# Kernel tuning notes

Measured on AMD Instinct MI355X. Metric: run time of the kernel, lower is better.

The kernel has to match this reference:

```python
import jax, jax.numpy as jnp
import numpy as np

B, CIN, H, W = 8, 128, 32, 32
COUT, K, STRIDE, PAD = 128, 3, 1, 1
DK, DV, NH = 64, 64, 8
DKH, DVH = DK // NH, DV // NH


def conv2d(x, w, b, stride, pad):
    out = jax.lax.conv_general_dilated(
        x, w, (stride, stride), [(pad, pad), (pad, pad)],
        dimension_numbers=("NCHW", "OIHW", "NCHW"))
    return out + b[None, :, None, None]


def rel_to_abs(x):
    # x: (b, Nh, L, 2L-1) relative -> (b, Nh, L, L) absolute via pad/reshape/slice
    b, nh, L, _ = x.shape
    x = jnp.pad(x, ((0, 0), (0, 0), (0, 0), (0, 1)))          # (b,Nh,L,2L)
    flat = x.reshape(b, nh, L * 2 * L)
    flat = jnp.pad(flat, ((0, 0), (0, 0), (0, L - 1)))
    final = flat.reshape(b, nh, L + 1, 2 * L - 1)
    return final[:, :, :L, L - 1:]


def relative_logits_1d(q, key_rel, Hh, Ww, Nh, case):
    # q: (b, Nh, x, y, dkh); key_rel: (2*len-1, dkh)
    rel = jnp.einsum("bhxyd,md->bhxym", q, key_rel)
    rel = rel.reshape(-1, Nh * Hh, Ww, 2 * Ww - 1)
    rel = rel_to_abs(rel)
    rel = rel.reshape(-1, Nh, Hh, Ww, Ww)
    rel = jnp.tile(rel[:, :, :, None, :, :], (1, 1, 1, Hh, 1, 1))  # (b,Nh,H,H,W,W)
    if case == "h":
        # torch .transpose(2,4).transpose(3,5)
        rel = rel.transpose(0, 1, 4, 5, 2, 3)
    return rel.reshape(-1, Nh, Hh * Ww, Hh * Ww)


def reference(x, w_general, b_general, w_qkv, b_qkv, w_out, b_out, key_rel_h, key_rel_w):
    batch, _, height, width = x.shape
    conv_out = conv2d(x, w_general, b_general, STRIDE, PAD)

    qkv = conv2d(x, w_qkv, b_qkv, 1, 0)
    q, k, v = jnp.split(qkv, [DK, 2 * DK], axis=1)
    # split heads: (B, Nh, c//Nh, H, W)
    q = q.reshape(batch, NH, DKH, height, width)
    k = k.reshape(batch, NH, DKH, height, width)
    v = v.reshape(batch, NH, DVH, height, width)
    # faithful to original bug: q / dkh**(-0.5) == q * sqrt(dkh)
    q = q / (DKH ** (-0.5))

    flat_q = q.reshape(batch, NH, height * width, DKH)
    flat_k = k.reshape(batch, NH, height * width, DKH)
    flat_v = v.reshape(batch, NH, height * width, DVH)

    logits = jnp.einsum("bhnd,bhmd->bhnm", flat_q, flat_k)

    # relative position logits
    q5 = q.transpose(0, 1, 3, 4, 2)  # (B, Nh, H, W, dkh)
    logits = logits + relative_logits_1d(q5, key_rel_h, height, width, NH, "h")
    logits = logits + relative_logits_1d(q5.transpose(0, 1, 3, 2, 4), key_rel_w, height, width, NH, "w")

    weights = jax.nn.softmax(logits, axis=-1)
    attn = jnp.einsum("bhnm,bhmd->bhnd", weights, flat_v)
    attn = attn.reshape(batch, NH, height, width, DVH)
    # combine heads: (B, Nh*dvh, H, W)
    attn = attn.transpose(0, 1, 4, 2, 3).reshape(batch, NH * DVH, height, width)
    attn = conv2d(attn, w_out, b_out, STRIDE, PAD)
    return jnp.concatenate((conv_out, attn), axis=1)


def setup_inputs():
    key = jax.random.key(0)
    ks = jax.random.split(key, 8)
    f = jnp.float32
    x = jax.random.normal(ks[0], (B, CIN, H, W), f)
    w_general = jax.random.normal(ks[1], (COUT - DV, CIN, K, K), f) * 0.02
    b_general = jnp.zeros((COUT - DV,), f)
    w_qkv = jax.random.normal(ks[2], (2 * DK + DV, CIN, 1, 1), f) * 0.05
    b_qkv = jnp.zeros((2 * DK + DV,), f)
    w_out = jax.random.normal(ks[3], (DV, DV, K, K), f) * 0.05
    b_out = jnp.zeros((DV,), f)
    key_rel_h = jax.random.normal(ks[4], (2 * H - 1, DKH), f)
    key_rel_w = jax.random.normal(ks[5], (2 * W - 1, DKH), f)
    return {"x": x, "w_general": w_general, "b_general": b_general,
            "w_qkv": w_qkv, "b_qkv": b_qkv, "w_out": w_out, "b_out": b_out,
            "key_rel_h": key_rel_h, "key_rel_w": key_rel_w}
```

## Files before the change

kernel.cpp:

```cpp
#include <hip/hip_runtime.h>
#include <hip/hip_bf16.h>


#define NP 1024
#define QSCALE 2.8284271247461903f
#define LOG2E  1.4426950408889634f

using bf16 = __hip_bfloat16;
typedef unsigned short ushort;
typedef unsigned int uint;
using bf16x8 = __attribute__((ext_vector_type(8))) short;
using f32x4  = __attribute__((ext_vector_type(4))) float;
using f32x2  = __attribute__((ext_vector_type(2))) float;

__device__ __forceinline__ float b2f(bf16 v) { return __bfloat162float(v); }
__device__ __forceinline__ ushort f2b(float v) {
  bf16 h = __float2bfloat16(v);
  ushort u; __builtin_memcpy(&u, &h, 2); return u;
}
__device__ __forceinline__ f32x2 up2(uint u) {
  f32x2 r;
  r[0] = __uint_as_float(u << 16);
  r[1] = __uint_as_float(u & 0xffff0000u);
  return r;
}

__device__ __forceinline__ float dot8(const float* a, const float* b) {
  float s = a[0] * b[0];
  s = fmaf(a[1], b[1], s); s = fmaf(a[2], b[2], s); s = fmaf(a[3], b[3], s);
  s = fmaf(a[4], b[4], s); s = fmaf(a[5], b[5], s); s = fmaf(a[6], b[6], s);
  s = fmaf(a[7], b[7], s);
  return s;
}

__device__ __forceinline__ int fenc(float f) { int i = __float_as_int(f); return i < 0 ? (i ^ 0x7fffffff) : i; }
__device__ __forceinline__ float fdec(int i) { return __int_as_float(i < 0 ? (i ^ 0x7fffffff) : i); }

#if defined(__has_builtin)
#if __has_builtin(__builtin_amdgcn_exp2f)
#define EXP2F __builtin_amdgcn_exp2f
#else
#define EXP2F exp2f
#endif
#else
#define EXP2F exp2f
#endif

#define OFF_QBUF   0
#define OFF_KB16   524288
#define OFF_VTB    786432
#define OFF_XPB    1310720
#define OFF_APB    1902592
#define OFF_WGB    2198528
#define OFF_WOB    2235392
#define OFF_BG     2253824
#define OFF_BQKV   2253888
#define OFF_BO     2254080
#define OFF_KRH    2254144
#define OFF_KRW    2254648
#define OFF_FLAG   2255152
#define OFF_WQB    2255168

__global__ __launch_bounds__(256) void cvt_kernel(
    const void* __restrict__ p0, const void* __restrict__ p1, const void* __restrict__ p2,
    const void* __restrict__ p3, const void* __restrict__ p4, const void* __restrict__ p5,
    const void* __restrict__ p6, const void* __restrict__ p7, const void* __restrict__ p8,
    float* __restrict__ ws, int* __restrict__ flag)
{
  __shared__ int partial[4];
  __shared__ uint lds[64][65];
  int t = threadIdx.x;
  const unsigned* xraw = (const unsigned*)p0;
  int cnt = 0;
  for (int i = t; i < 1024; i += 256) {
    unsigned elo = (xraw[i] >> 7) & 0xffu;
    cnt += (elo >= 64u && elo <= 133u) ? 1 : 0;
  }
#pragma unroll
  for (int off = 1; off < 64; off <<= 1) cnt += __shfl_xor(cnt, off);
  if ((t & 63) == 0) partial[t >> 6] = cnt;
  __syncthreads();
  int tot = partial[0] + partial[1] + partial[2] + partial[3];
  int f32 = (tot >= 650) ? 0 : 1;
  if (blockIdx.x == 0 && t == 0) *flag = f32;

  int gsz = gridDim.x * 256;
  int gid = blockIdx.x * 256 + t;

  const void* src[5] = {p2, p4, p6, p7, p8};
  const int   n[5]    = {64, 192, 64, 504, 504};
  const int   doff[5] = {OFF_BG, OFF_BQKV, OFF_BO, OFF_KRH, OFF_KRW};
#pragma unroll
  for (int s = 0; s < 5; s++) {
    float* dst = ws + doff[s];
    if (f32) { const float* sp = (const float*)src[s];
      for (int i = gid; i < n[s]; i += gsz) dst[i] = sp[i];
    } else { const bf16* sp = (const bf16*)src[s];
      for (int i = gid; i < n[s]; i += gsz) dst[i] = b2f(sp[i]);
    }
  }

  {
    float4* z = (float4*)(ws + OFF_VTB);
    for (int i = gid; i < 131072; i += gsz) z[i] = float4{0.f, 0.f, 0.f, 0.f};
  }

  {
    uint4 z = {0u, 0u, 0u, 0u};
    uint4* xp = (uint4*)(ws + OFF_XPB);
    uint4* ap = (uint4*)(ws + OFF_APB);
    for (int s = gid; s < 9248; s += gsz) {
      int pb = s / 1156, rem = s - pb * 1156;
      int y = rem / 34, x = rem - y * 34;
      if (y == 0 || y == 33 || x == 0 || x == 33) {
        uint4* d1 = xp + (size_t)s * 16;
#pragma unroll
        for (int k = 0; k < 16; k++) d1[k] = z;
        uint4* d2 = ap + (size_t)s * 8;
#pragma unroll
        for (int k = 0; k < 8; k++) d2[k] = z;
      }
    }
  }

  {
    ushort* wgb = (ushort*)(ws + OFF_WGB);
    for (int s = gid; s < 73728; s += gsz) {
      int kykx = s >> 13, co = (s >> 7) & 63, ci = s & 127;
      int si = (co * 128 + ci) * 9 + kykx;
      wgb[s] = f32 ? f2b(((const float*)p1)[si]) : ((const ushort*)p1)[si];
    }
  }
  {
    ushort* wob = (ushort*)(ws + OFF_WOB);
    for (int s = gid; s < 36864; s += gsz) {
      int kykx = s >> 12, co = (s >> 6) & 63, ci = s & 63;
      int si = (co * 64 + ci) * 9 + kykx;
      wob[s] = f32 ? f2b(((const float*)p5)[si]) : ((const ushort*)p5)[si];
    }
  }
  {
    ushort* wqb = (ushort*)(ws + OFF_WQB);
    for (int s = gid; s < 24576; s += gsz) {
      wqb[s] = f32 ? f2b(((const float*)p3)[s]) : ((const ushort*)p3)[s];
    }
  }

  if (blockIdx.x < 128) {
    int w = t >> 6, lane = t & 63;
    int b = blockIdx.x >> 4;
    int pp0 = (blockIdx.x & 15) * 64;
    if (f32) {
      const float* xs = (const float*)p0 + (size_t)b * 131072 + pp0;
#pragma unroll 4
      for (int i = 0; i < 16; i++) {
        int cp = w * 16 + i;
        float v0 = xs[(size_t)(2 * cp) * 1024 + lane];
        float v1 = xs[(size_t)(2 * cp + 1) * 1024 + lane];
        lds[cp][lane] = (uint)f2b(v0) | ((uint)f2b(v1) << 16);
      }
    } else {
      const ushort* xs = (const ushort*)p0 + (size_t)b * 131072 + pp0;
#pragma unroll 4
      for (int i = 0; i < 16; i++) {
        int cp = w * 16 + i;
        uint v0 = xs[(size_t)(2 * cp) * 1024 + lane];
        uint v1 = xs[(size_t)(2 * cp + 1) * 1024 + lane];
        lds[cp][lane] = v0 | (v1 << 16);
      }
    }
    __syncthreads();
    uint* xp32 = (uint*)(ws + OFF_XPB);
#pragma unroll 4
    for (int i = 0; i < 16; i++) {
      int p = w * 16 + i;
      int pp = pp0 + p;
      int y = pp >> 5, x = pp & 31;
      xp32[((size_t)(b * 34 + y + 1) * 34 + x + 1) * 64 + lane] = lds[lane][p];
    }
  }
}

__global__ __launch_bounds__(256) void qkv_mfma_kernel(
    const ushort* __restrict__ xp, const ushort* __restrict__ wqb,
    const float* __restrict__ bias, float* __restrict__ qbuf,
    ushort* __restrict__ kb16, ushort* __restrict__ vtb)
{
  int pt = blockIdx.x;
  int b  = blockIdx.y;
  int lane = threadIdx.x & 63;
  int w = threadIdx.x >> 6;
  int n = lane & 15;
  int kg = lane >> 4;
  int p0 = pt * 16;
  int px = p0 + n;
  int y = px >> 5, x = px & 31;

  const ushort* bbase = xp + ((size_t)(b * 34 + y + 1) * 34 + (x + 1)) * 128 + kg * 8;
  bf16x8 Bf[4];
#pragma unroll
  for (int c = 0; c < 4; c++) Bf[c] = *(const bf16x8*)(bbase + c * 32);

  f32x4 acc0 = {0.f, 0.f, 0.f, 0.f};
  f32x4 acc1 = {0.f, 0.f, 0.f, 0.f};
  f32x4 acc2 = {0.f, 0.f, 0.f, 0.f};
  {
    const ushort* abase = wqb + (size_t)(w * 16 + n) * 128 + kg * 8;
#pragma unroll
    for (int c = 0; c < 4; c++) {
      bf16x8 A = *(const bf16x8*)(abase + c * 32);
      acc0 = __builtin_amdgcn_mfma_f32_16x16x32_bf16(A, Bf[c], acc0, 0, 0, 0);
    }
  }
  {
    const ushort* abase = wqb + (size_t)((w + 4) * 16 + n) * 128 + kg * 8;
#pragma unroll
    for (int c = 0; c < 4; c++) {
      bf16x8 A = *(const bf16x8*)(abase + c * 32);
      acc1 = __builtin_amdgcn_mfma_f32_16x16x32_bf16(A, Bf[c], acc1, 0, 0, 0);
    }
  }
  {
    const ushort* abase = wqb + (size_t)((w + 8) * 16 + n) * 128 + kg * 8;
#pragma unroll
    for (int c = 0; c < 4; c++) {
      bf16x8 A = *(const bf16x8*)(abase + c * 32);
      acc2 = __builtin_amdgcn_mfma_f32_16x16x32_bf16(A, Bf[c], acc2, 0, 0, 0);
    }
  }

#pragma unroll
  for (int r = 0; r < 4; r++) {
    int co = w * 16 + kg * 4 + r;
    float v = acc0[r] + bias[co];
    qbuf[((size_t)b * 64 + co) * NP + px] = v * QSCALE;
  }
#pragma unroll
  for (int r = 0; r < 4; r++) {
    int co = (w + 4) * 16 + kg * 4 + r;
    float v = acc1[r] + bias[co];
    kb16[((size_t)b * 64 + (co - 64)) * NP + px] = f2b(v);
  }
#pragma unroll
  for (int r = 0; r < 4; r++) {
    int co = (w + 8) * 16 + kg * 4 + r;
    float v = acc2[r] + bias[co];
    int ch = co - 128;
    int h = ch >> 3;
    int d0 = px & 7;
    int m  = (ch & 7) * 128 + (px >> 3);
    vtb[((size_t)(b * 8 + h) * 16 + d0) * 1024 + m] = f2b(v);
  }
}

template <int CINT>
__device__ __forceinline__ void conv_body(
    const ushort* __restrict__ xp, const ushort* __restrict__ wp,
    const float* __restrict__ bias, void* __restrict__ out,
    int co_base, const int* __restrict__ flag, int pt, int b)
{
  int lane = threadIdx.x & 63;
  int w = threadIdx.x >> 6;
  int n = lane & 15;
  int kg = lane >> 4;
  int p0 = pt * 16;
  int y = p0 >> 5, x0 = p0 & 31;

  const ushort* abase = wp + (size_t)(w * 16 + n) * CINT + kg * 8;
  const ushort* bbase = xp + ((size_t)(b * 34 + y) * 34 + x0 + n) * CINT + kg * 8;

  f32x4 acc0 = {0.f, 0.f, 0.f, 0.f};
  f32x4 acc1 = {0.f, 0.f, 0.f, 0.f};
#pragma unroll
  for (int c = 0; c < CINT / 32; c++) {
    int ci0 = c * 32;
#pragma unroll
    for (int kp = 0; kp < 9; kp++) {
      int ky = kp / 3, kx = kp - ky * 3;
      bf16x8 A = *(const bf16x8*)(abase + (size_t)kp * 64 * CINT + ci0);
      bf16x8 B = *(const bf16x8*)(bbase + (size_t)(ky * 34 + kx) * CINT + ci0);
      if (kp & 1) acc1 = __builtin_amdgcn_mfma_f32_16x16x32_bf16(A, B, acc1, 0, 0, 0);
      else        acc0 = __builtin_amdgcn_mfma_f32_16x16x32_bf16(A, B, acc0, 0, 0, 0);
    }
  }

  int f32o = *flag;
#pragma unroll
  for (int r = 0; r < 4; r++) {
    int co = w * 16 + kg * 4 + r;
    float v = acc0[r] + acc1[r] + bias[co];
    size_t eoff = ((size_t)b * 128 + co_base + co) * 1024 + p0 + n;
    if (f32o) ((float*)out)[eoff] = v;
    else ((bf16*)out)[eoff] = __float2bfloat16(v);
  }
}

__global__ __launch_bounds__(256, 4) void attn_conv_kernel(
    const float* __restrict__ qbuf, const ushort* __restrict__ kb16, const ushort* __restrict__ vtb,
    const float* __restrict__ krh, const float* __restrict__ krw,
    ushort* __restrict__ apb,
    const ushort* __restrict__ xp, const ushort* __restrict__ wgb,
    const float* __restrict__ bg, void* __restrict__ out, const int* __restrict__ flag)
{
  int bx = blockIdx.x;
  if (bx >= 1024) {
    int id = bx - 1024;
    conv_body<128>(xp, wgb, bg, out, 0, flag, id & 63, id >> 6);
    return;
  }

  __shared__ float bw2[2][NP];
  __shared__ float bhT[2][32][32];
  __shared__ float qsT[2][32][8];
  __shared__ __align__(16) float krhs[64][12];
  __shared__ __align__(16) float krws[64][12];
  __shared__ ushort Plds[4][16][40];
  __shared__ float lred[4][16];
  __shared__ int smax[3];

  int t = threadIdx.x;
  int cp = bx & 15, h = (bx >> 4) & 7, b = bx >> 7;
  int C0 = cp * 2;
  const float* qbase = qbuf + ((size_t)b * 64 + h * 8) * NP;
  const uint4* kb4 = (const uint4*)(kb16 + ((size_t)b * 64 + h * 8) * NP);
  const ushort* vth = vtb + (size_t)(b * 8 + h) * 16384;

  if (t < 3) smax[t] = (t == 0) ? 0 : fenc(-3.0e38f);

  for (int idx = t; idx < 63 * 8; idx += 256) {
    krhs[idx >> 3][idx & 7] = krh[idx];
    krws[idx >> 3][idx & 7] = krw[idx];
  }
  for (int idx = t; idx < 512; idx += 256) {
    int cs = idx >> 8, d = (idx >> 5) & 7, r = idx & 31;
    qsT[cs][r][d] = qbase[(size_t)d * NP + r * 32 + (C0 + cs)];
  }
  float kn2 = 0.f;
#pragma unroll
  for (int rr = 0; rr < 4; rr++) {
    uint4 ku = kb4[rr * 256 + t];
    f32x2 k0 = up2(ku.x), k1 = up2(ku.y), k2 = up2(ku.z), k3 = up2(ku.w);
    f32x2 s2 = k0 * k0;
    s2 = __builtin_elementwise_fma(k1, k1, s2);
    s2 = __builtin_elementwise_fma(k2, k2, s2);
    s2 = __builtin_elementwise_fma(k3, k3, s2);
    kn2 = fmaxf(kn2, s2[0] + s2[1]);
  }
  __syncthreads();
  atomicMax(&smax[0], __float_as_int(kn2));

  float bwm = -3.0e38f;
  for (int idx = t; idx < 2048; idx += 256) {
    int cs = idx >> 10, m = idx & 1023;
    int rg = m >> 5, j2 = m & 31;
    float s = dot8(qsT[cs][rg], krws[j2 - rg + 31]) * LOG2E;
    bw2[cs][m] = s;
    bwm = fmaxf(bwm, s);
  }
  float bhm = -3.0e38f;
  for (int idx = t; idx < 2048; idx += 256) {
    int cs = idx >> 10, r = idx & 1023;
    int i = r >> 5, J = r & 31;
    float s = dot8(qsT[cs][i], krhs[J - (C0 + cs) + 31]) * LOG2E;
    bhT[cs][i][J] = s;
    bhm = fmaxf(bhm, s);
  }
  atomicMax(&smax[1], fenc(bwm));
  atomicMax(&smax[2], fenc(bhm));
  __syncthreads();

  float kmaxn = sqrtf(__int_as_float(smax[0]));
  float bmax = fdec(smax[1]) + fdec(smax[2]);

  int w = t >> 6, lane = t & 63;
  int quad = lane >> 4, nIdx = lane & 15;
  int n0 = cp * 64 + w * 16;
  int nQ = n0 + nIdx;
  int Cs = w >> 1;
  int J = ((w & 1) << 4) + nIdx;

  const bf16x8 zero8 = {0, 0, 0, 0, 0, 0, 0, 0};

  const float* qrow = qbase + (size_t)nQ * 8;
  bf16x8 Bq = zero8;
  float nn = 0.f;
  ushort ub[8];
#pragma unroll
  for (int d = 0; d < 8; d++) {
    float v = qrow[d] * LOG2E;
    ub[d] = f2b(v);
    float vr = __uint_as_float((uint)ub[d] << 16);
    nn = fmaf(vr, vr, nn);
  }
  if (quad == 0) {
#pragma unroll
    for (int d = 0; d < 8; d++) Bq[d] = (short)ub[d];
  }
  float Mn = sqrtf(nn) * kmaxn + bmax;

  f32x4 accO = {0.f, 0.f, 0.f, 0.f};
  float lpart = 0.f;
  ushort* prow = &Plds[w][nIdx][0];

#pragma unroll 2
  for (int mc = 0; mc < 32; ++mc) {
    int mb = mc * 32;
    float pre = bhT[Cs][mc][J] - Mn;
    ushort pb[8];
#pragma unroll
    for (int s = 0; s < 2; ++s) {
      int mt = mb + s * 16;
      bf16x8 Ak = *(const bf16x8*)(kb4 + mt + nIdx);
      if (quad != 0) Ak = zero8;
      f32x4 S = __builtin_amdgcn_mfma_f32_16x16x32_bf16(Ak, Bq, f32x4{0.f,0.f,0.f,0.f}, 0, 0, 0);
      float4 bw4 = *(const float4*)&bw2[Cs][mt + (quad << 2)];
      const float bwv[4] = {bw4.x, bw4.y, bw4.z, bw4.w};
#pragma unroll
      for (int r = 0; r < 4; ++r) {
        float p = EXP2F(S[r] + bwv[r] + pre);
        lpart += p;
        pb[s * 4 + r] = f2b(p);
      }
    }
    uint2 w0, w1;
    w0.x = (uint)pb[0] | ((uint)pb[1] << 16);
    w0.y = (uint)pb[2] | ((uint)pb[3] << 16);
    w1.x = (uint)pb[4] | ((uint)pb[5] << 16);
    w1.y = (uint)pb[6] | ((uint)pb[7] << 16);
    *(uint2*)(prow + (quad << 2))        = w0;
    *(uint2*)(prow + 16 + (quad << 2))   = w1;
    bf16x8 Ap = *(const bf16x8*)(prow + (quad << 3));
    bf16x8 Bv = *(const bf16x8*)(vth + (size_t)nIdx * 1024 + mb + (quad << 3));
    accO = __builtin_amdgcn_mfma_f32_16x16x32_bf16(Ap, Bv, accO, 0, 0, 0);
  }

  lpart += __shfl_xor(lpart, 16);
  lpart += __shfl_xor(lpart, 32);
  if (lane < 16) lred[w][lane] = lpart;
  float4 lr4 = *(const float4*)&lred[w][quad << 2];
  const float lr[4] = {lr4.x, lr4.y, lr4.z, lr4.w};

  if (nIdx < 8) {
#pragma unroll
    for (int r = 0; r < 4; ++r) {
      int n = n0 + (quad << 2) + r;
      float v = accO[r] / lr[r];
      apb[((size_t)(b * 34 + (n >> 5) + 1) * 34 + (n & 31) + 1) * 64 + h * 8 + nIdx] = f2b(v);
    }
  }
}

template <int CINT>
__global__ __launch_bounds__(256) void conv_mfma_kernel(
    const ushort* __restrict__ xp, const ushort* __restrict__ wp,
    const float* __restrict__ bias, void* __restrict__ out,
    int co_base, const int* __restrict__ flag)
{
  conv_body<CINT>(xp, wp, bias, out, co_base, flag, blockIdx.x, blockIdx.y);
}

extern "C" void kernel_launch(void* const* d_in, const int* in_sizes, int n_in,
                              void* d_out, int out_size, void* d_ws, size_t ws_size,
                              hipStream_t stream) {
  float* ws = (float*)d_ws;
  float*  qbuf  = ws + OFF_QBUF;
  ushort* kb16  = (ushort*)(ws + OFF_KB16);
  ushort* vtb   = (ushort*)(ws + OFF_VTB);
  ushort* xpb   = (ushort*)(ws + OFF_XPB);
  ushort* apb   = (ushort*)(ws + OFF_APB);
  ushort* wgb   = (ushort*)(ws + OFF_WGB);
  ushort* wob   = (ushort*)(ws + OFF_WOB);
  ushort* wqb   = (ushort*)(ws + OFF_WQB);
  float*  bgf   = ws + OFF_BG;
  float*  bqkvf = ws + OFF_BQKV;
  float*  bof   = ws + OFF_BO;
  float*  krhf  = ws + OFF_KRH;
  float*  krwf  = ws + OFF_KRW;
  int*    flag  = (int*)(ws + OFF_FLAG);

  cvt_kernel<<<512, 256, 0, stream>>>(d_in[0], d_in[1], d_in[2], d_in[3], d_in[4],
                                      d_in[5], d_in[6], d_in[7], d_in[8], ws, flag);
  qkv_mfma_kernel<<<dim3(64, 8), 256, 0, stream>>>(xpb, wqb, bqkvf, qbuf, kb16, vtb);
  attn_conv_kernel<<<1536, 256, 0, stream>>>(qbuf, kb16, vtb, krhf, krwf, apb,
                                             xpb, wgb, bgf, d_out, flag);
  conv_mfma_kernel<64><<<dim3(64, 8), 256, 0, stream>>>(apb, wob, bof, d_out, 64, flag);
}
```

Measured before the change: 142.7 us.

## Feed P straight from registers into 16x16x16 MFMAs, dropping the LDS round-trip

```diff
diff --git a/kernel.cpp b/kernel.cpp
--- a/kernel.cpp
+++ b/kernel.cpp
@@ -10,6 +10,7 @@
 typedef unsigned short ushort;
 typedef unsigned int uint;
 using bf16x8 = __attribute__((ext_vector_type(8))) short;
+using bf16x4 = __attribute__((ext_vector_type(4))) short;
 using f32x4  = __attribute__((ext_vector_type(4))) float;
 using f32x2  = __attribute__((ext_vector_type(2))) float;
 
@@ -44,6 +45,23 @@
 #endif
 #else
 #define EXP2F exp2f
+#endif
+
+#if defined(__has_builtin)
+#if __has_builtin(__builtin_amdgcn_mfma_f32_16x16x16_bf16)
+#define MFMA16(A,B,C) __builtin_amdgcn_mfma_f32_16x16x16_bf16(A,B,C,0,0,0)
+#elif __has_builtin(__builtin_amdgcn_mfma_f32_16x16x16bf16_1k)
+#define MFMA16(A,B,C) __builtin_amdgcn_mfma_f32_16x16x16bf16_1k(A,B,C,0,0,0)
+#endif
+#endif
+#ifndef MFMA16
+__device__ __forceinline__ f32x4 mfma16_asm(bf16x4 a, bf16x4 b, f32x4 c) {
+  f32x4 d;
+  asm volatile("v_mfma_f32_16x16x16_bf16 %0, %1, %2, %3"
+               : "=v"(d) : "v"(a), "v"(b), "v"(c));
+  return d;
+}
+#define MFMA16(A,B,C) mfma16_asm(A,B,C)
 #endif
 
 #define OFF_QBUF   0
@@ -98,11 +116,6 @@
     } else { const bf16* sp = (const bf16*)src[s];
       for (int i = gid; i < n[s]; i += gsz) dst[i] = b2f(sp[i]);
     }
-  }
-
-  {
-    float4* z = (float4*)(ws + OFF_VTB);
-    for (int i = gid; i < 131072; i += gsz) z[i] = float4{0.f, 0.f, 0.f, 0.f};
   }
 
   {
@@ -314,7 +327,6 @@
   __shared__ float qsT[2][32][8];
   __shared__ __align__(16) float krhs[64][12];
   __shared__ __align__(16) float krws[64][12];
-  __shared__ ushort Plds[4][16][40];
   __shared__ float lred[4][16];
   __shared__ int smax[3];
 
@@ -331,9 +343,11 @@
     krhs[idx >> 3][idx & 7] = krh[idx];
     krws[idx >> 3][idx & 7] = krw[idx];
   }
-  for (int idx = t; idx < 512; idx += 256) {
-    int cs = idx >> 8, d = (idx >> 5) & 7, r = idx & 31;
-    qsT[cs][r][d] = qbase[(size_t)d * NP + r * 32 + (C0 + cs)];
+  {
+    int d = t >> 5, r = t & 31;
+    float2 qv = *(const float2*)(qbase + (size_t)d * NP + r * 32 + C0);
+    qsT[0][r][d] = qv.x;
+    qsT[1][r][d] = qv.y;
   }
   float kn2 = 0.f;
 #pragma unroll
@@ -400,38 +414,37 @@
 
   f32x4 accO = {0.f, 0.f, 0.f, 0.f};
   float lpart = 0.f;
-  ushort* prow = &Plds[w][nIdx][0];
+  const uint4* krow = kb4 + nIdx;
+  const ushort* vrow = vth + (size_t)nIdx * 1024 + (quad << 2);
 
 #pragma unroll 2
   for (int mc = 0; mc < 32; ++mc) {
     int mb = mc * 32;
     float pre = bhT[Cs][mc][J] - Mn;
-    ushort pb[8];
-#pragma unroll
-    for (int s = 0; s < 2; ++s) {
-      int mt = mb + s * 16;
-      bf16x8 Ak = *(const bf16x8*)(kb4 + mt + nIdx);
-      if (quad != 0) Ak = zero8;
-      f32x4 S = __builtin_amdgcn_mfma_f32_16x16x32_bf16(Ak, Bq, f32x4{0.f,0.f,0.f,0.f}, 0, 0, 0);
-      float4 bw4 = *(const float4*)&bw2[Cs][mt + (quad << 2)];
-      const float bwv[4] = {bw4.x, bw4.y, bw4.z, bw4.w};
-#pragma unroll
-      for (int r = 0; r < 4; ++r) {
-        float p = EXP2F(S[r] + bwv[r] + pre);
-        lpart += p;
-        pb[s * 4 + r] = f2b(p);
-      }
-    }
-    uint2 w0, w1;
-    w0.x = (uint)pb[0] | ((uint)pb[1] << 16);
-    w0.y = (uint)pb[2] | ((uint)pb[3] << 16);
-    w1.x = (uint)pb[4] | ((uint)pb[5] << 16);
-    w1.y = (uint)pb[6] | ((uint)pb[7] << 16);
-    *(uint2*)(prow + (quad << 2))        = w0;
-    *(uint2*)(prow + 16 + (quad << 2))   = w1;
-    bf16x8 Ap = *(const bf16x8*)(prow + (quad << 3));
-    bf16x8 Bv = *(const bf16x8*)(vth + (size_t)nIdx * 1024 + mb + (quad << 3));
-    accO = __builtin_amdgcn_mfma_f32_16x16x32_bf16(Ap, Bv, accO, 0, 0, 0);
+    bf16x8 a0 = *(const bf16x8*)(krow + mb);
+    bf16x8 a1 = *(const bf16x8*)(krow + mb + 16);
+    uint2 v0u = *(const uint2*)(vrow + mb);
+    uint2 v1u = *(const uint2*)(vrow + mb + 16);
+    f32x4 S0 = __builtin_amdgcn_mfma_f32_16x16x32_bf16(a0, Bq, f32x4{0.f,0.f,0.f,0.f}, 0, 0, 0);
+    f32x4 S1 = __builtin_amdgcn_mfma_f32_16x16x32_bf16(a1, Bq, f32x4{0.f,0.f,0.f,0.f}, 0, 0, 0);
+    float4 bwA = *(const float4*)&bw2[Cs][mb + (quad << 2)];
+    float4 bwB = *(const float4*)&bw2[Cs][mb + 16 + (quad << 2)];
+    float p0 = EXP2F(S0[0] + bwA.x + pre);
+    float p1 = EXP2F(S0[1] + bwA.y + pre);
+    float p2 = EXP2F(S0[2] + bwA.z + pre);
+    float p3 = EXP2F(S0[3] + bwA.w + pre);
+    float p4 = EXP2F(S1[0] + bwB.x + pre);
+    float p5 = EXP2F(S1[1] + bwB.y + pre);
+    float p6 = EXP2F(S1[2] + bwB.z + pre);
+    float p7 = EXP2F(S1[3] + bwB.w + pre);
+    lpart += ((p0 + p1) + (p2 + p3)) + ((p4 + p5) + (p6 + p7));
+    uint2 ua, ub2;
+    ua.x  = (uint)f2b(p0) | ((uint)f2b(p1) << 16);
+    ua.y  = (uint)f2b(p2) | ((uint)f2b(p3) << 16);
+    ub2.x = (uint)f2b(p4) | ((uint)f2b(p5) << 16);
+    ub2.y = (uint)f2b(p6) | ((uint)f2b(p7) << 16);
+    accO = MFMA16(__builtin_bit_cast(bf16x4, ua),  __builtin_bit_cast(bf16x4, v0u), accO);
+    accO = MFMA16(__builtin_bit_cast(bf16x4, ub2), __builtin_bit_cast(bf16x4, v1u), accO);
   }
 
   lpart += __shfl_xor(lpart, 16);
```

Result: slower. 162.6 us (+14.0%).

## Fold softmax denominator into PV MFMA via ones column in V

Applied to the files above, without the earlier changes.

```diff
diff --git a/kernel.cpp b/kernel.cpp
--- a/kernel.cpp
+++ b/kernel.cpp
@@ -101,8 +101,11 @@
   }
 
   {
-    float4* z = (float4*)(ws + OFF_VTB);
-    for (int i = gid; i < 131072; i += gsz) z[i] = float4{0.f, 0.f, 0.f, 0.f};
+    uint* vo = (uint*)(ws + OFF_VTB);
+    for (int i = gid; i < 32768; i += gsz) {
+      int head = i >> 9, mw = i & 511;
+      vo[head * 8192 + 4096 + mw] = 0x3F803F80u;
+    }
   }
 
   {
@@ -311,12 +314,12 @@
 
   __shared__ float bw2[2][NP];
   __shared__ float bhT[2][32][32];
-  __shared__ float qsT[2][32][8];
-  __shared__ __align__(16) float krhs[64][12];
-  __shared__ __align__(16) float krws[64][12];
-  __shared__ ushort Plds[4][16][40];
-  __shared__ float lred[4][16];
+  __shared__ __align__(16) char qpun[5120];
+  __shared__ float krhs[64][8];
+  __shared__ float krws[64][8];
   __shared__ int smax[3];
+  float (*qsT)[32][8]   = (float (*)[32][8])qpun;
+  ushort (*Plds)[16][40] = (ushort (*)[16][40])qpun;
 
   int t = threadIdx.x;
   int cp = bx & 15, h = (bx >> 4) & 7, b = bx >> 7;
@@ -331,9 +334,11 @@
     krhs[idx >> 3][idx & 7] = krh[idx];
     krws[idx >> 3][idx & 7] = krw[idx];
   }
-  for (int idx = t; idx < 512; idx += 256) {
-    int cs = idx >> 8, d = (idx >> 5) & 7, r = idx & 31;
-    qsT[cs][r][d] = qbase[(size_t)d * NP + r * 32 + (C0 + cs)];
+  {
+    int d = t >> 5, r = t & 31;
+    float2 qv = *(const float2*)(qbase + (size_t)d * NP + r * 32 + C0);
+    qsT[0][r][d] = qv.x;
+    qsT[1][r][d] = qv.y;
   }
   float kn2 = 0.f;
 #pragma unroll
@@ -399,7 +404,6 @@
   float Mn = sqrtf(nn) * kmaxn + bmax;
 
   f32x4 accO = {0.f, 0.f, 0.f, 0.f};
-  float lpart = 0.f;
   ushort* prow = &Plds[w][nIdx][0];
 
 #pragma unroll 2
@@ -411,14 +415,12 @@
     for (int s = 0; s < 2; ++s) {
       int mt = mb + s * 16;
       bf16x8 Ak = *(const bf16x8*)(kb4 + mt + nIdx);
-      if (quad != 0) Ak = zero8;
       f32x4 S = __builtin_amdgcn_mfma_f32_16x16x32_bf16(Ak, Bq, f32x4{0.f,0.f,0.f,0.f}, 0, 0, 0);
       float4 bw4 = *(const float4*)&bw2[Cs][mt + (quad << 2)];
       const float bwv[4] = {bw4.x, bw4.y, bw4.z, bw4.w};
 #pragma unroll
       for (int r = 0; r < 4; ++r) {
         float p = EXP2F(S[r] + bwv[r] + pre);
-        lpart += p;
         pb[s * 4 + r] = f2b(p);
       }
     }
@@ -434,11 +436,10 @@
     accO = __builtin_amdgcn_mfma_f32_16x16x32_bf16(Ap, Bv, accO, 0, 0, 0);
   }
 
-  lpart += __shfl_xor(lpart, 16);
-  lpart += __shfl_xor(lpart, 32);
-  if (lane < 16) lred[w][lane] = lpart;
-  float4 lr4 = *(const float4*)&lred[w][quad << 2];
-  const float lr[4] = {lr4.x, lr4.y, lr4.z, lr4.w};
+  int srcl = (lane & 48) | 8;
+  float lr[4];
+#pragma unroll
+  for (int r = 0; r < 4; ++r) lr[r] = __shfl(accO[r], srcl);
 
   if (nIdx < 8) {
 #pragma unroll
```

After: 149.7 us. 4.9% more time.
